# Kernel tuning notes

Hardware: AMD Instinct MI355X
Metric: run time of the kernel (lower is better)

Reference implementation:

```python
import jax, jax.numpy as jnp
import numpy as np

DT_MIN, DT_MAX = 1e-3, 0.1
DT_RANK, D_STATE = 64, 16


def setup_inputs() -> dict:
    key = jax.random.key(0)
    ks = jax.random.split(key, 8)
    B, L, D_MODEL, D_INNER = 2, 4096, 1024, 2048
    s = 0.02
    return {
        "x": jax.random.normal(ks[0], (B, L, D_MODEL), jnp.float32),
        "W_in": jax.random.normal(ks[1], (D_MODEL, 2 * D_INNER), jnp.float32) * s,
        "W_xproj": jax.random.normal(ks[2], (D_INNER, DT_RANK + 2 * D_STATE), jnp.float32) * s,
        "W_dt": jax.random.normal(ks[3], (DT_RANK, D_INNER), jnp.float32) * s,
        "b_dt": jax.random.normal(ks[4], (D_INNER,), jnp.float32) * s,
        "A_log": jnp.log(jax.random.uniform(ks[5], (D_INNER, D_STATE), jnp.float32) + 0.5),
        "D": jnp.ones((D_INNER,), jnp.float32),
        "W_out": jax.random.normal(ks[6], (D_INNER, D_MODEL), jnp.float32) * s,
    }


def _selective_scan(xp, delta, A, Bm, Cm):
    # xp, delta: [B, L, d_inner]; Bm, Cm: [B, L, d_state]; A: [d_inner, d_state]
    batch, L, d_inner = xp.shape
    d_state = A.shape[1]

    def step(h, inp):
        x_t, dt_t, B_t, C_t = inp  # [B,di], [B,di], [B,ds], [B,ds]
        A_bar = 1.0 + A[None] * dt_t[..., None]            # [B, di, ds]
        B_bar = B_t[:, None, :] * dt_t[..., None]          # [B, di, ds]
        h = A_bar * h + B_bar * x_t[..., None]             # [B, di, ds]
        y_t = jnp.sum(C_t[:, None, :] * h, axis=-1)        # [B, di]
        return h, y_t

    h0 = jnp.zeros((batch, d_inner, d_state), xp.dtype)
    xs = (
        jnp.swapaxes(xp, 0, 1),
        jnp.swapaxes(delta, 0, 1),
        jnp.swapaxes(Bm, 0, 1),
        jnp.swapaxes(Cm, 0, 1),
    )
    _, ys = jax.lax.scan(step, h0, xs)  # ys: [L, B, d_inner]
    return jnp.swapaxes(ys, 0, 1)


def reference(x, W_in, W_xproj, W_dt, b_dt, A_log, D, W_out):
    xz = x @ W_in
    xp, z = jnp.split(xz, 2, axis=-1)                      # [B,L,d_inner] each
    x_dbl = xp @ W_xproj
    dlt, Bm, Cm = jnp.split(x_dbl, [DT_RANK, DT_RANK + D_STATE], axis=-1)
    delta = jnp.clip(jax.nn.softplus(dlt @ W_dt + b_dt), DT_MIN, DT_MAX)
    A = -jnp.exp(A_log)
    y = _selective_scan(xp, delta, A, Bm, Cm)
    y = y + D[None, None, :] * xp
    y = y * jax.nn.silu(z)
    return y @ W_out
```

## Files before the change

kernel.cpp:

```cpp
#include <hip/hip_runtime.h>
#include <cstdint>
#include <cstddef>

typedef unsigned short u16;
typedef __attribute__((ext_vector_type(8))) short bf16x8;
typedef __attribute__((ext_vector_type(4))) float f32x4;

__device__ __forceinline__ float bf2f(u16 u) {
  unsigned v = ((unsigned)u) << 16;
  return __builtin_bit_cast(float, v);
}
__device__ __forceinline__ u16 f2bf(float f) {
  unsigned u = __builtin_bit_cast(unsigned, f);
  u = (u + 0x7FFFu + ((u >> 16) & 1u)) >> 16;
  return (u16)u;
}

__device__ __forceinline__ void gload16(const void* g, void* l) {
  __builtin_amdgcn_global_load_lds(
      (const __attribute__((address_space(1))) void*)g,
      (__attribute__((address_space(3))) void*)l,
      16, 0, 0);
}

__device__ __forceinline__ int swz(int lb) { return lb ^ (((lb >> 7) & 7) << 4); }

__global__ __launch_bounds__(256) void f32_to_bf16_kernel(
    const float* __restrict__ in, u16* __restrict__ out, int n) {
  int i = (blockIdx.x * 256 + threadIdx.x) * 4;
  if (i < n) {
    float4 v = *(const float4*)(in + i);
    ushort4 o;
    o.x = f2bf(v.x); o.y = f2bf(v.y); o.z = f2bf(v.z); o.w = f2bf(v.w);
    *(ushort4*)(out + i) = o;
  }
}

__global__ void transpose_f32_bf16T_kernel(
    const float* __restrict__ in, u16* __restrict__ out, int R, int C) {
  __shared__ float tile[32][33];
  const int bx = blockIdx.x * 32;
  const int by = blockIdx.y * 32;
  const int tx = threadIdx.x, ty = threadIdx.y;
#pragma unroll
  for (int i = 0; i < 32; i += 8)
    tile[ty + i][tx] = in[(size_t)(by + ty + i) * C + bx + tx];
  __syncthreads();
#pragma unroll
  for (int i = 0; i < 32; i += 8)
    out[(size_t)(bx + ty + i) * R + by + tx] = f2bf(tile[tx][ty + i]);
}

template <int BN, int EPI>
__global__ __launch_bounds__(512, 2) void gemm256(
    const u16* __restrict__ Ap, const u16* __restrict__ Btp,
    int M, int N, int K, int gx,
    void* __restrict__ o0, void* __restrict__ o1) {
  constexpr int NFR = BN / 64;
  constexpr int NFH = NFR / 2;
  constexpr int B_ISS = BN / 64;
  constexpr int BH = B_ISS / 2;
  constexpr int WN = BN / 4;
  constexpr int HSH = (BN == 256) ? 5 : 4;
  constexpr int AREG = 32768;
  constexpr int BREG = BN * 128;
  constexpr int BUFSZ = AREG + BREG;
  __shared__ __align__(1024) char smem[2 * BUFSZ];

  const int tid = threadIdx.x;
  const int wid = tid >> 6, lane = tid & 63;
  const int wr = wid >> 2, wc = wid & 3;
  const int l16 = lane & 15, lk = lane >> 4;

  const int nwg = gridDim.x, bid = blockIdx.x;
  const int rb = (bid & 7) * (nwg >> 3) + (bid >> 3);
  const int bx = rb % gx, by = rb / gx;
  const int m0 = by * 256, n0 = bx * BN;

  const u16* gA[4];
  const u16* gB[B_ISS];
#pragma unroll
  for (int i = 0; i < 4; ++i) {
    int lb = swz(i * 8192 + tid * 16);
    gA[i] = Ap + (size_t)(m0 + (lb >> 7)) * K + ((lb & 127) >> 1);
  }
#pragma unroll
  for (int i = 0; i < B_ISS; ++i) {
    int lb = swz(i * 8192 + tid * 16);
    int rl = lb >> 7;
    int half = (rl >= BN / 2) ? 1 : 0;
    int r = rl & (BN / 2 - 1);
    int n = ((r >> HSH) << (HSH + 1)) + (half << HSH) + (r & ((1 << HSH) - 1));
    gB[i] = Btp + (size_t)(n0 + n) * K + ((lb & 127) >> 1);
  }

  auto stageA = [&](int kt, int h) {
    char* dst = smem + (kt & 1) * BUFSZ + (wid << 10);
    gload16(gA[h] + kt * 64, dst + h * 8192);
    gload16(gA[h + 2] + kt * 64, dst + (h + 2) * 8192);
  };
  auto stageB = [&](int kt, int h) {
    char* dst = smem + (kt & 1) * BUFSZ + AREG + (wid << 10);
#pragma unroll
    for (int j = 0; j < BH; ++j)
      gload16(gB[h * BH + j] + kt * 64, dst + (h * BH + j) * 8192);
  };

  auto offA = [&](int f, int kk) {
    return swz((wr * 128 + f * 16 + l16) * 128 + kk * 64 + lk * 16);
  };
  auto offB = [&](int nf, int kk) {
    int rl = (nf >= NFH ? BN / 2 : 0) + wc * (WN / 2) + (nf % NFH) * 16 + l16;
    return swz(rl * 128 + kk * 64 + lk * 16);
  };

  f32x4 acc[8][NFR];
#pragma unroll
  for (int f = 0; f < 8; ++f)
#pragma unroll
    for (int n = 0; n < NFR; ++n) {
      f32x4 z = {0.f, 0.f, 0.f, 0.f};
      acc[f][n] = z;
    }

  const int NT = K >> 6;
  stageA(0, 0); stageB(0, 0); stageA(0, 1); stageB(0, 1);
  if constexpr (BH == 2) asm volatile("s_waitcnt vmcnt(4)" ::: "memory");
  else                   asm volatile("s_waitcnt vmcnt(3)" ::: "memory");
  __builtin_amdgcn_s_barrier();

  for (int kt = 0; kt < NT; ++kt) {
    const char* bufA = smem + (kt & 1) * BUFSZ;
    const char* bufB = bufA + AREG;
    bf16x8 af[4][2], bh[2][NFH][2];

#pragma unroll
    for (int j = 0; j < 4; ++j)
#pragma unroll
      for (int kk = 0; kk < 2; ++kk)
        af[j][kk] = *(const bf16x8*)(bufA + offA(j, kk));
#pragma unroll
    for (int j = 0; j < NFH; ++j)
#pragma unroll
      for (int kk = 0; kk < 2; ++kk)
        bh[0][j][kk] = *(const bf16x8*)(bufB + offB(j, kk));
    if (kt + 1 < NT) stageA(kt + 1, 0);
    __builtin_amdgcn_s_barrier();
    asm volatile("s_waitcnt lgkmcnt(0)" ::: "memory");
    __builtin_amdgcn_sched_barrier(0);
    __builtin_amdgcn_s_setprio(1);
#pragma unroll
    for (int j = 0; j < 4; ++j)
#pragma unroll
      for (int n2 = 0; n2 < NFH; ++n2)
#pragma unroll
        for (int kk = 0; kk < 2; ++kk)
          acc[j][n2] = __builtin_amdgcn_mfma_f32_16x16x32_bf16(
              af[j][kk], bh[0][n2][kk], acc[j][n2], 0, 0, 0);
    __builtin_amdgcn_s_setprio(0);
    if (kt + 1 < NT) asm volatile("s_waitcnt vmcnt(2)" ::: "memory");
    else             asm volatile("s_waitcnt vmcnt(0)" ::: "memory");
    __builtin_amdgcn_s_barrier();

#pragma unroll
    for (int j = 0; j < NFH; ++j)
#pragma unroll
      for (int kk = 0; kk < 2; ++kk)
        bh[1][j][kk] = *(const bf16x8*)(bufB + offB(NFH + j, kk));
    if (kt + 1 < NT) stageB(kt + 1, 0);
    __builtin_amdgcn_s_barrier();
    asm volatile("s_waitcnt lgkmcnt(0)" ::: "memory");
    __builtin_amdgcn_sched_barrier(0);
    __builtin_amdgcn_s_setprio(1);
#pragma unroll
    for (int j = 0; j < 4; ++j)
#pragma unroll
      for (int n2 = 0; n2 < NFH; ++n2)
#pragma unroll
        for (int kk = 0; kk < 2; ++kk)
          acc[j][NFH + n2] = __builtin_amdgcn_mfma_f32_16x16x32_bf16(
              af[j][kk], bh[1][n2][kk], acc[j][NFH + n2], 0, 0, 0);
    __builtin_amdgcn_s_setprio(0);
    __builtin_amdgcn_s_barrier();

#pragma unroll
    for (int j = 0; j < 4; ++j)
#pragma unroll
      for (int kk = 0; kk < 2; ++kk)
        af[j][kk] = *(const bf16x8*)(bufA + offA(4 + j, kk));
    if (kt + 1 < NT) { stageA(kt + 1, 1); stageB(kt + 1, 1); }
    __builtin_amdgcn_s_barrier();
    asm volatile("s_waitcnt lgkmcnt(0)" ::: "memory");
    __builtin_amdgcn_sched_barrier(0);
    __builtin_amdgcn_s_setprio(1);
#pragma unroll
    for (int j = 0; j < 4; ++j)
#pragma unroll
      for (int n2 = 0; n2 < NFH; ++n2)
#pragma unroll
        for (int kk = 0; kk < 2; ++kk)
          acc[4 + j][NFH + n2] = __builtin_amdgcn_mfma_f32_16x16x32_bf16(
              af[j][kk], bh[1][n2][kk], acc[4 + j][NFH + n2], 0, 0, 0);
    __builtin_amdgcn_s_setprio(0);
    __builtin_amdgcn_s_barrier();

    __builtin_amdgcn_s_setprio(1);
#pragma unroll
    for (int j = 0; j < 4; ++j)
#pragma unroll
      for (int n2 = 0; n2 < NFH; ++n2)
#pragma unroll
        for (int kk = 0; kk < 2; ++kk)
          acc[4 + j][n2] = __builtin_amdgcn_mfma_f32_16x16x32_bf16(
              af[j][kk], bh[0][n2][kk], acc[4 + j][n2], 0, 0, 0);
    __builtin_amdgcn_s_setprio(0);
    if (kt + 1 < NT) {
      if constexpr (BH == 2) asm volatile("s_waitcnt vmcnt(4)" ::: "memory");
      else                   asm volatile("s_waitcnt vmcnt(3)" ::: "memory");
    }
    __builtin_amdgcn_s_barrier();
  }

#pragma unroll
  for (int f = 0; f < 8; ++f) {
#pragma unroll
    for (int n = 0; n < NFR; ++n) {
#pragma unroll
      for (int rr = 0; rr < 4; ++rr) {
        const int row = m0 + wr * 128 + f * 16 + lk * 4 + rr;
        const int col = n0 + wc * WN + n * 16 + l16;
        float v = acc[f][n][rr];
        if constexpr (EPI == 0) {
          if (col < 2048) {
            ((u16*)o0)[(size_t)row * 2048 + col] = f2bf(v);
          } else {
            float sv = v / (1.f + __expf(-v));
            ((u16*)o1)[(size_t)row * 2048 + (col - 2048)] = f2bf(sv);
          }
        } else {
          ((float*)o0)[(size_t)row * (size_t)N + col] = v;
        }
      }
    }
  }
}

template <int BN, int NR, int EPI>
__global__ __launch_bounds__(256) void gemm_bt(
    const u16* __restrict__ A, const u16* __restrict__ Bt,
    int M, int N, int K, int KS,
    void* __restrict__ o0, const float* __restrict__ bias) {
  constexpr int BM = 128, BK = 32, MR = 4;
  __shared__ __align__(16) u16 As[BM * BK];
  __shared__ __align__(16) u16 Bs[BN * BK];
  const int tid = threadIdx.x;
  const int wid = tid >> 6, lane = tid & 63;
  const int wr = wid >> 1, wc = wid & 1;
  const int m0 = blockIdx.y * BM, n0 = blockIdx.x * BN;
  const int l16 = lane & 15, lk = lane >> 4;

  f32x4 acc[MR][NR];
#pragma unroll
  for (int m = 0; m < MR; ++m)
#pragma unroll
    for (int n = 0; n < NR; ++n) {
      f32x4 z = {0.f, 0.f, 0.f, 0.f};
      acc[m][n] = z;
    }

  constexpr int CH_A = (BM * BK * 2) / 1024;
  constexpr int CH_B = (BN * BK * 2) / 1024;

  const int kbeg = blockIdx.z * KS, kend = kbeg + KS;
  for (int k0 = kbeg; k0 < kend; k0 += BK) {
    for (int c = wid; c < CH_A; c += 4) {
      int off = c * 1024 + lane * 16;
      int e = off >> 1;
      int m = e >> 5, kk = e & 31;
      gload16(A + (size_t)(m0 + m) * K + (k0 + kk), (char*)As + off);
    }
    for (int c = wid; c < CH_B; c += 4) {
      int off = c * 1024 + lane * 16;
      int e = off >> 1;
      int n = e >> 5, kk = e & 31;
      gload16(Bt + (size_t)(n0 + n) * K + (k0 + kk), (char*)Bs + off);
    }
    __syncthreads();
    bf16x8 af[MR], bfr[NR];
#pragma unroll
    for (int m = 0; m < MR; ++m)
      af[m] = *(const bf16x8*)(As + (wr * 64 + m * 16 + l16) * BK + lk * 8);
#pragma unroll
    for (int n = 0; n < NR; ++n)
      bfr[n] = *(const bf16x8*)(Bs + (wc * (NR * 16) + n * 16 + l16) * BK + lk * 8);
#pragma unroll
    for (int m = 0; m < MR; ++m)
#pragma unroll
      for (int n = 0; n < NR; ++n)
        acc[m][n] = __builtin_amdgcn_mfma_f32_16x16x32_bf16(af[m], bfr[n], acc[m][n], 0, 0, 0);
    __syncthreads();
  }

#pragma unroll
  for (int m = 0; m < MR; ++m) {
#pragma unroll
    for (int n = 0; n < NR; ++n) {
#pragma unroll
      for (int r = 0; r < 4; ++r) {
        const int row = m0 + wr * 64 + m * 16 + (lane >> 4) * 4 + r;
        const int col = n0 + wc * (NR * 16) + n * 16 + (lane & 15);
        float v = acc[m][n][r];
        if constexpr (EPI == 2) {
          v += bias[col];
          float sp = (v > 20.f) ? v : log1pf(__expf(v));
          sp = fminf(fmaxf(sp, 1e-3f), 0.1f);
          ((u16*)o0)[(size_t)row * 2048 + col] = f2bf(sp);
        } else {
          ((float*)o0)[((size_t)blockIdx.z * M + row) * 96 + col] = v;
        }
      }
    }
  }
}

__global__ __launch_bounds__(256) void reduce_xdbl(
    const float* __restrict__ part, u16* __restrict__ dlt,
    float* __restrict__ Bc, float* __restrict__ Cc) {
  int idx = blockIdx.x * 256 + threadIdx.x;
  int row = idx / 24, c4 = idx % 24;
  const float* p = part + (size_t)row * 96 + c4 * 4;
  f32x4 v = *(const f32x4*)p;
#pragma unroll
  for (int z = 1; z < 4; ++z)
    v += *(const f32x4*)(p + (size_t)z * 8192 * 96);
  int col = c4 * 4;
  if (col < 64) {
    ushort4 o;
    o.x = f2bf(v[0]); o.y = f2bf(v[1]); o.z = f2bf(v[2]); o.w = f2bf(v[3]);
    *(ushort4*)(dlt + (size_t)row * 64 + col) = o;
  } else if (col < 80) {
    *(f32x4*)(Bc + (size_t)row * 16 + (col - 64)) = v;
  } else {
    *(f32x4*)(Cc + (size_t)row * 16 + (col - 80)) = v;
  }
}

template <int TC>
__global__ __launch_bounds__(256) void scan_pass1(
    const u16* __restrict__ xp, const u16* __restrict__ dt,
    const float* __restrict__ Bc, const float* __restrict__ A_log,
    float* __restrict__ P, float* __restrict__ Q, int NC) {
  const int di = blockIdx.x * 256 + threadIdx.x;
  const int c = blockIdx.y, b = blockIdx.z;
  __shared__ __align__(16) float Bs[TC * 16];
  {
    const float* src = Bc + (size_t)(b * 4096 + c * TC) * 16;
    for (int i = threadIdx.x; i < TC * 4; i += 256)
      *(float4*)(Bs + i * 4) = *(const float4*)(src + i * 4);
  }
  float A[16], h[16], Pp[16];
#pragma unroll
  for (int s = 0; s < 16; ++s) {
    A[s] = -__expf(A_log[di * 16 + s]);
    h[s] = 0.f;
    Pp[s] = 1.f;
  }
  __syncthreads();
  size_t gidx = (size_t)(b * 4096 + c * TC) * 2048 + di;
  for (int t = 0; t < TC; ++t, gidx += 2048) {
    float xv = bf2f(xp[gidx]), dv = bf2f(dt[gidx]);
    float dvx = dv * xv;
#pragma unroll
    for (int q = 0; q < 4; ++q) {
      f32x4 bv = ((const f32x4*)(Bs + t * 16))[q];
#pragma unroll
      for (int j = 0; j < 4; ++j) {
        int s = q * 4 + j;
        float abar = fmaf(A[s], dv, 1.f);
        h[s] = fmaf(abar, h[s], bv[j] * dvx);
        Pp[s] *= abar;
      }
    }
  }
  const size_t obase = ((size_t)(b * NC + c) * 16) * 2048 + di;
#pragma unroll
  for (int s = 0; s < 16; ++s) {
    P[obase + (size_t)s * 2048] = Pp[s];
    Q[obase + (size_t)s * 2048] = h[s];
  }
}

__global__ __launch_bounds__(256) void scan_pass2(
    const float* __restrict__ P, const float* __restrict__ Q,
    float* __restrict__ Hin, int NC) {
  const int di = blockIdx.x * 256 + threadIdx.x;
  const int s = blockIdx.y, b = blockIdx.z;
  float hin = 0.f;
  const size_t idx0 = ((size_t)(b * NC) * 16 + s) * 2048 + di;
#pragma unroll 8
  for (int c = 0; c < NC; ++c) {
    size_t idx = idx0 + (size_t)c * (16 * 2048);
    Hin[idx] = hin;
    hin = fmaf(P[idx], hin, Q[idx]);
  }
}

template <int TC>
__global__ __launch_bounds__(256) void scan_pass3(
    const u16* __restrict__ xp, const u16* __restrict__ dt,
    const u16* __restrict__ zs, const float* __restrict__ Bc,
    const float* __restrict__ Cc, const float* __restrict__ A_log,
    const float* __restrict__ Dv, const float* __restrict__ Hin,
    u16* __restrict__ Y, int NC) {
  const int di = blockIdx.x * 256 + threadIdx.x;
  const int c = blockIdx.y, b = blockIdx.z;
  __shared__ __align__(16) float Bs[TC * 16], Cs[TC * 16];
  {
    const float* srcB = Bc + (size_t)(b * 4096 + c * TC) * 16;
    const float* srcC = Cc + (size_t)(b * 4096 + c * TC) * 16;
    for (int i = threadIdx.x; i < TC * 4; i += 256) {
      *(float4*)(Bs + i * 4) = *(const float4*)(srcB + i * 4);
      *(float4*)(Cs + i * 4) = *(const float4*)(srcC + i * 4);
    }
  }
  float A[16], h[16];
  const size_t hbase = ((size_t)(b * NC + c) * 16) * 2048 + di;
#pragma unroll
  for (int s = 0; s < 16; ++s) {
    A[s] = -__expf(A_log[di * 16 + s]);
    h[s] = Hin[hbase + (size_t)s * 2048];
  }
  const float Dg = Dv[di];
  __syncthreads();
  size_t gidx = (size_t)(b * 4096 + c * TC) * 2048 + di;
  for (int t = 0; t < TC; ++t, gidx += 2048) {
    float xv = bf2f(xp[gidx]), dv = bf2f(dt[gidx]), zv = bf2f(zs[gidx]);
    float dvx = dv * xv;
    float y = 0.f;
#pragma unroll
    for (int q = 0; q < 4; ++q) {
      f32x4 bv = ((const f32x4*)(Bs + t * 16))[q];
      f32x4 cv = ((const f32x4*)(Cs + t * 16))[q];
#pragma unroll
      for (int j = 0; j < 4; ++j) {
        int s = q * 4 + j;
        float abar = fmaf(A[s], dv, 1.f);
        h[s] = fmaf(abar, h[s], bv[j] * dvx);
        y = fmaf(cv[j], h[s], y);
      }
    }
    float yo = fmaf(Dg, xv, y) * zv;
    Y[gidx] = f2bf(yo);
  }
}

extern "C" void kernel_launch(void* const* d_in, const int* in_sizes, int n_in,
                              void* d_out, int out_size, void* d_ws, size_t ws_size,
                              hipStream_t stream) {
  (void)in_sizes; (void)n_in; (void)out_size; (void)ws_size;
  const float* x       = (const float*)d_in[0];
  const float* W_in    = (const float*)d_in[1];
  const float* W_xproj = (const float*)d_in[2];
  const float* W_dt    = (const float*)d_in[3];
  const float* b_dt    = (const float*)d_in[4];
  const float* A_log   = (const float*)d_in[5];
  const float* Dv      = (const float*)d_in[6];
  const float* W_out   = (const float*)d_in[7];
  float* out = (float*)d_out;

  constexpr size_t MB = 1ull << 20;
  char* ws = (char*)d_ws;
  constexpr size_t O_XP    = 0;
  constexpr size_t O_ZS    = 32 * MB;
  constexpr size_t O_DELTA = 64 * MB;
  constexpr size_t O_BC    = 96 * MB;
  constexpr size_t O_CC    = O_BC + 512 * 1024;
  constexpr size_t O_WOUTT = 97 * MB;
  constexpr size_t O_Y     = 101 * MB;
  constexpr size_t O_XB    = 133 * MB;
  constexpr size_t O_WINT  = 149 * MB;
  constexpr size_t O_WXT   = 157 * MB;
  constexpr size_t O_WDTT  = O_WXT + 393216;
  constexpr size_t O_DLT   = O_WDTT + 262144;
  constexpr size_t O_P     = 133 * MB;
  constexpr size_t O_Q     = 149 * MB;
  constexpr size_t O_HIN   = 165 * MB;
  constexpr size_t O_XDP   = O_P;

  u16* xb    = (u16*)(ws + O_XB);
  u16* WinT  = (u16*)(ws + O_WINT);
  u16* WxT   = (u16*)(ws + O_WXT);
  u16* WdtT  = (u16*)(ws + O_WDTT);
  u16* WoutT = (u16*)(ws + O_WOUTT);
  u16* xpb   = (u16*)(ws + O_XP);
  u16* zsb   = (u16*)(ws + O_ZS);
  u16* dltb  = (u16*)(ws + O_DLT);
  float* Bcf = (float*)(ws + O_BC);
  float* Ccf = (float*)(ws + O_CC);
  u16* delb  = (u16*)(ws + O_DELTA);
  u16* Yb    = (u16*)(ws + O_Y);
  float* Pf  = (float*)(ws + O_P);
  float* Qf  = (float*)(ws + O_Q);
  float* Hin = (float*)(ws + O_HIN);
  float* xdp = (float*)(ws + O_XDP);

  dim3 tb(32, 8);
  f32_to_bf16_kernel<<<8192 * 1024 / 1024, 256, 0, stream>>>(x, xb, 8192 * 1024);
  transpose_f32_bf16T_kernel<<<dim3(4096 / 32, 1024 / 32), tb, 0, stream>>>(W_in, WinT, 1024, 4096);
  transpose_f32_bf16T_kernel<<<dim3(96 / 32, 2048 / 32), tb, 0, stream>>>(W_xproj, WxT, 2048, 96);
  transpose_f32_bf16T_kernel<<<dim3(2048 / 32, 64 / 32), tb, 0, stream>>>(W_dt, WdtT, 64, 2048);
  transpose_f32_bf16T_kernel<<<dim3(1024 / 32, 2048 / 32), tb, 0, stream>>>(W_out, WoutT, 2048, 1024);

  gemm256<256, 0><<<512, 512, 0, stream>>>(
      xb, WinT, 8192, 4096, 1024, 16, xpb, zsb);
  gemm_bt<96, 3, 4><<<dim3(1, 8192 / 128, 4), 256, 0, stream>>>(
      xpb, WxT, 8192, 96, 2048, 512, xdp, nullptr);
  reduce_xdbl<<<8192 * 24 / 256, 256, 0, stream>>>(xdp, dltb, Bcf, Ccf);
  gemm_bt<128, 4, 2><<<dim3(2048 / 128, 8192 / 128, 1), 256, 0, stream>>>(
      dltb, WdtT, 8192, 2048, 64, 64, delb, b_dt);

  constexpr int NC = 64, TC = 64;
  scan_pass1<TC><<<dim3(8, NC, 2), 256, 0, stream>>>(
      xpb, delb, Bcf, A_log, Pf, Qf, NC);
  scan_pass2<<<dim3(8, 16, 2), 256, 0, stream>>>(Pf, Qf, Hin, NC);
  scan_pass3<TC><<<dim3(8, NC, 2), 256, 0, stream>>>(
      xpb, delb, zsb, Bcf, Ccf, A_log, Dv, Hin, Yb, NC);

  gemm256<128, 3><<<256, 512, 0, stream>>>(
      Yb, WoutT, 8192, 1024, 2048, 8, out, nullptr);
}
```

Before: 328.0 us.

## Process two channels per thread in scan passes and reorder GEMM tile raster

The scan pass1 and pass3 kernels now give each thread two adjacent d_inner channels. They load bf16 pairs as 32-bit words, store P/Q/Hin as float2 and write Y as packed bf16 pairs, and the scan grids are halved to match. The GEMM block index mapping is switched from column-major to row-major over M tiles (gy parameter), which changes which tiles run concurrently and so their L2 reuse. The scan change widens memory accesses and adds per-thread ILP, at the cost of half as many threads and more registers for these latency-bound scan kernels.

Measured after the change: 339.5 us. +3.5%, slower.

```diff
diff --git a/kernel.cpp b/kernel.cpp
--- a/kernel.cpp
+++ b/kernel.cpp
@@ -14,6 +14,9 @@
   unsigned u = __builtin_bit_cast(unsigned, f);
   u = (u + 0x7FFFu + ((u >> 16) & 1u)) >> 16;
   return (u16)u;
+}
+__device__ __forceinline__ unsigned f2bf2(float lo, float hi) {
+  return (unsigned)f2bf(lo) | ((unsigned)f2bf(hi) << 16);
 }
 
 __device__ __forceinline__ void gload16(const void* g, void* l) {
@@ -54,7 +57,7 @@
 template <int BN, int EPI>
 __global__ __launch_bounds__(512, 2) void gemm256(
     const u16* __restrict__ Ap, const u16* __restrict__ Btp,
-    int M, int N, int K, int gx,
+    int M, int N, int K, int gy,
     void* __restrict__ o0, void* __restrict__ o1) {
   constexpr int NFR = BN / 64;
   constexpr int NFH = NFR / 2;
@@ -74,7 +77,7 @@
 
   const int nwg = gridDim.x, bid = blockIdx.x;
   const int rb = (bid & 7) * (nwg >> 3) + (bid >> 3);
-  const int bx = rb % gx, by = rb / gx;
+  const int by = rb % gy, bx = rb / gy;
   const int m0 = by * 256, n0 = bx * BN;
 
   const u16* gA[4];
@@ -350,7 +353,7 @@
     const u16* __restrict__ xp, const u16* __restrict__ dt,
     const float* __restrict__ Bc, const float* __restrict__ A_log,
     float* __restrict__ P, float* __restrict__ Q, int NC) {
-  const int di = blockIdx.x * 256 + threadIdx.x;
+  const int di0 = (blockIdx.x * 256 + threadIdx.x) * 2;
   const int c = blockIdx.y, b = blockIdx.z;
   __shared__ __align__(16) float Bs[TC * 16];
   {
@@ -358,35 +361,43 @@
     for (int i = threadIdx.x; i < TC * 4; i += 256)
       *(float4*)(Bs + i * 4) = *(const float4*)(src + i * 4);
   }
-  float A[16], h[16], Pp[16];
+  float A[2][16], h[2][16], Pp[2][16];
+#pragma unroll
+  for (int u = 0; u < 2; ++u)
+#pragma unroll
+    for (int s = 0; s < 16; ++s) {
+      A[u][s] = -__expf(A_log[(di0 + u) * 16 + s]);
+      h[u][s] = 0.f;
+      Pp[u][s] = 1.f;
+    }
+  __syncthreads();
+  size_t gidx = (size_t)(b * 4096 + c * TC) * 2048 + di0;
+  for (int t = 0; t < TC; ++t, gidx += 2048) {
+    unsigned x2 = *(const unsigned*)(xp + gidx);
+    unsigned d2 = *(const unsigned*)(dt + gidx);
+    float xv[2] = {bf2f((u16)x2), bf2f((u16)(x2 >> 16))};
+    float dv[2] = {bf2f((u16)d2), bf2f((u16)(d2 >> 16))};
+#pragma unroll
+    for (int u = 0; u < 2; ++u) {
+      float dvx = dv[u] * xv[u];
+#pragma unroll
+      for (int q = 0; q < 4; ++q) {
+        f32x4 bv = ((const f32x4*)(Bs + t * 16))[q];
+#pragma unroll
+        for (int j = 0; j < 4; ++j) {
+          int s = q * 4 + j;
+          float abar = fmaf(A[u][s], dv[u], 1.f);
+          h[u][s] = fmaf(abar, h[u][s], bv[j] * dvx);
+          Pp[u][s] *= abar;
+        }
+      }
+    }
+  }
+  const size_t obase = ((size_t)(b * NC + c) * 16) * 2048 + di0;
 #pragma unroll
   for (int s = 0; s < 16; ++s) {
-    A[s] = -__expf(A_log[di * 16 + s]);
-    h[s] = 0.f;
-    Pp[s] = 1.f;
-  }
-  __syncthreads();
-  size_t gidx = (size_t)(b * 4096 + c * TC) * 2048 + di;
-  for (int t = 0; t < TC; ++t, gidx += 2048) {
-    float xv = bf2f(xp[gidx]), dv = bf2f(dt[gidx]);
-    float dvx = dv * xv;
-#pragma unroll
-    for (int q = 0; q < 4; ++q) {
-      f32x4 bv = ((const f32x4*)(Bs + t * 16))[q];
-#pragma unroll
-      for (int j = 0; j < 4; ++j) {
-        int s = q * 4 + j;
-        float abar = fmaf(A[s], dv, 1.f);
-        h[s] = fmaf(abar, h[s], bv[j] * dvx);
-        Pp[s] *= abar;
-      }
-    }
-  }
-  const size_t obase = ((size_t)(b * NC + c) * 16) * 2048 + di;
-#pragma unroll
-  for (int s = 0; s < 16; ++s) {
-    P[obase + (size_t)s * 2048] = Pp[s];
-    Q[obase + (size_t)s * 2048] = h[s];
+    *(float2*)(P + obase + (size_t)s * 2048) = make_float2(Pp[0][s], Pp[1][s]);
+    *(float2*)(Q + obase + (size_t)s * 2048) = make_float2(h[0][s], h[1][s]);
   }
 }
 
@@ -412,7 +423,7 @@
     const float* __restrict__ Cc, const float* __restrict__ A_log,
     const float* __restrict__ Dv, const float* __restrict__ Hin,
     u16* __restrict__ Y, int NC) {
-  const int di = blockIdx.x * 256 + threadIdx.x;
+  const int di0 = (blockIdx.x * 256 + threadIdx.x) * 2;
   const int c = blockIdx.y, b = blockIdx.z;
   __shared__ __align__(16) float Bs[TC * 16], Cs[TC * 16];
   {
@@ -423,34 +434,49 @@
       *(float4*)(Cs + i * 4) = *(const float4*)(srcC + i * 4);
     }
   }
-  float A[16], h[16];
-  const size_t hbase = ((size_t)(b * NC + c) * 16) * 2048 + di;
+  float A[2][16], h[2][16];
+  const size_t hbase = ((size_t)(b * NC + c) * 16) * 2048 + di0;
+#pragma unroll
+  for (int u = 0; u < 2; ++u)
+#pragma unroll
+    for (int s = 0; s < 16; ++s)
+      A[u][s] = -__expf(A_log[(di0 + u) * 16 + s]);
 #pragma unroll
   for (int s = 0; s < 16; ++s) {
-    A[s] = -__expf(A_log[di * 16 + s]);
-    h[s] = Hin[hbase + (size_t)s * 2048];
-  }
-  const float Dg = Dv[di];
+    float2 hv = *(const float2*)(Hin + hbase + (size_t)s * 2048);
+    h[0][s] = hv.x;
+    h[1][s] = hv.y;
+  }
+  const float Dg0 = Dv[di0], Dg1 = Dv[di0 + 1];
   __syncthreads();
-  size_t gidx = (size_t)(b * 4096 + c * TC) * 2048 + di;
+  size_t gidx = (size_t)(b * 4096 + c * TC) * 2048 + di0;
   for (int t = 0; t < TC; ++t, gidx += 2048) {
-    float xv = bf2f(xp[gidx]), dv = bf2f(dt[gidx]), zv = bf2f(zs[gidx]);
-    float dvx = dv * xv;
-    float y = 0.f;
-#pragma unroll
-    for (int q = 0; q < 4; ++q) {
-      f32x4 bv = ((const f32x4*)(Bs + t * 16))[q];
-      f32x4 cv = ((const f32x4*)(Cs + t * 16))[q];
-#pragma unroll
-      for (int j = 0; j < 4; ++j) {
-        int s = q * 4 + j;
-        float abar = fmaf(A[s], dv, 1.f);
-        h[s] = fmaf(abar, h[s], bv[j] * dvx);
-        y = fmaf(cv[j], h[s], y);
+    unsigned x2 = *(const unsigned*)(xp + gidx);
+    unsigned d2 = *(const unsigned*)(dt + gidx);
+    unsigned z2 = *(const unsigned*)(zs + gidx);
+    float xv[2] = {bf2f((u16)x2), bf2f((u16)(x2 >> 16))};
+    float dv[2] = {bf2f((u16)d2), bf2f((u16)(d2 >> 16))};
+    float zv[2] = {bf2f((u16)z2), bf2f((u16)(z2 >> 16))};
+    float y[2] = {0.f, 0.f};
+#pragma unroll
+    for (int u = 0; u < 2; ++u) {
+      float dvx = dv[u] * xv[u];
+#pragma unroll
+      for (int q = 0; q < 4; ++q) {
+        f32x4 bv = ((const f32x4*)(Bs + t * 16))[q];
+        f32x4 cv = ((const f32x4*)(Cs + t * 16))[q];
+#pragma unroll
+        for (int j = 0; j < 4; ++j) {
+          int s = q * 4 + j;
+          float abar = fmaf(A[u][s], dv[u], 1.f);
+          h[u][s] = fmaf(abar, h[u][s], bv[j] * dvx);
+          y[u] = fmaf(cv[j], h[u][s], y[u]);
+        }
       }
     }
-    float yo = fmaf(Dg, xv, y) * zv;
-    Y[gidx] = f2bf(yo);
+    float yo0 = fmaf(Dg0, xv[0], y[0]) * zv[0];
+    float yo1 = fmaf(Dg1, xv[1], y[1]) * zv[1];
+    *(unsigned*)(Y + gidx) = f2bf2(yo0, yo1);
   }
 }
 
@@ -512,7 +538,7 @@
   transpose_f32_bf16T_kernel<<<dim3(1024 / 32, 2048 / 32), tb, 0, stream>>>(W_out, WoutT, 2048, 1024);
 
   gemm256<256, 0><<<512, 512, 0, stream>>>(
-      xb, WinT, 8192, 4096, 1024, 16, xpb, zsb);
+      xb, WinT, 8192, 4096, 1024, 32, xpb, zsb);
   gemm_bt<96, 3, 4><<<dim3(1, 8192 / 128, 4), 256, 0, stream>>>(
       xpb, WxT, 8192, 96, 2048, 512, xdp, nullptr);
   reduce_xdbl<<<8192 * 24 / 256, 256, 0, stream>>>(xdp, dltb, Bcf, Ccf);
@@ -520,12 +546,12 @@
       dltb, WdtT, 8192, 2048, 64, 64, delb, b_dt);
 
   constexpr int NC = 64, TC = 64;
-  scan_pass1<TC><<<dim3(8, NC, 2), 256, 0, stream>>>(
+  scan_pass1<TC><<<dim3(4, NC, 2), 256, 0, stream>>>(
       xpb, delb, Bcf, A_log, Pf, Qf, NC);
   scan_pass2<<<dim3(8, 16, 2), 256, 0, stream>>>(Pf, Qf, Hin, NC);
-  scan_pass3<TC><<<dim3(8, NC, 2), 256, 0, stream>>>(
+  scan_pass3<TC><<<dim3(4, NC, 2), 256, 0, stream>>>(
       xpb, delb, zsb, Bcf, Ccf, A_log, Dv, Hin, Yb, NC);
 
   gemm256<128, 3><<<256, 512, 0, stream>>>(
-      Yb, WoutT, 8192, 1024, 2048, 8, out, nullptr);
-}
+      Yb, WoutT, 8192, 1024, 2048, 32, out, nullptr);
+}
```
